# Kernel optimization log

Measured on AMD Instinct MI355X. Metric: run time of the kernel, lower is better.

The kernel has to match this reference:

```python
import jax, jax.numpy as jnp
import numpy as np


def _gcn_conv(x, src, dst, norm, W, b, n_nodes):
    # PyG GCNConv: transform then normalized scatter-add aggregation.
    h = x @ W                                        # [N, F_out]
    msg = h[src] * norm[:, None]                     # [E+N, F_out] gather
    out = jax.ops.segment_sum(msg, dst, num_segments=n_nodes)  # scatter-add
    return out + b


def setup_inputs() -> dict:
    key = jax.random.key(0)
    ks = jax.random.split(key, 8)
    N, E, F_in, H, C = 100000, 1000000, 128, 64, 40
    x = jax.random.normal(ks[0], (N, F_in), dtype=jnp.float32)
    edge_index = jax.random.randint(ks[1], (2, E), 0, N, dtype=jnp.int64)
    W1 = jax.random.normal(ks[2], (F_in, H), dtype=jnp.float32) * (1.0 / np.sqrt(F_in))
    b1 = jnp.zeros((H,), jnp.float32)
    W2 = jax.random.normal(ks[3], (H, H), dtype=jnp.float32) * (1.0 / np.sqrt(H))
    b2 = jnp.zeros((H,), jnp.float32)
    Wc = jax.random.normal(ks[4], (H, C), dtype=jnp.float32) * (1.0 / np.sqrt(H))
    bc = jnp.zeros((C,), jnp.float32)
    return {"x": x, "edge_index": edge_index, "W1": W1, "b1": b1,
            "W2": W2, "b2": b2, "Wc": Wc, "bc": bc}


def reference(x, edge_index, W1, b1, W2, b2, Wc, bc):
    n_nodes = x.shape[0]
    # Add self loops (GCNConv default), symmetric normalization.
    loop = jnp.arange(n_nodes, dtype=edge_index.dtype)
    src = jnp.concatenate([edge_index[0], loop])
    dst = jnp.concatenate([edge_index[1], loop])
    deg = jax.ops.segment_sum(jnp.ones_like(dst, jnp.float32), dst,
                              num_segments=n_nodes)
    dinv = jnp.where(deg > 0, jax.lax.rsqrt(jnp.maximum(deg, 1.0)), 0.0)
    norm = dinv[src] * dinv[dst]                     # [E+N]

    h = jax.nn.relu(_gcn_conv(x, src, dst, norm, W1, b1, n_nodes))
    # dropout: identity (inference / training=False)
    h = jax.nn.relu(_gcn_conv(h, src, dst, norm, W2, b2, n_nodes))
    return h @ Wc + bc                               # [N, out_dim]
```

## Files before the change

kernel.cpp:

```cpp
#include <hip/hip_runtime.h>
#include <hip/hip_fp16.h>


#define BUCKET_BITS  8
#define BUCKET_NODES 256
#define MAXB 512
#define CAP  8192
#define OFF_MASK 0x3FFFFF

typedef _Float16 half8 __attribute__((ext_vector_type(8)));
typedef float    f32x4 __attribute__((ext_vector_type(4)));

union H8  { uint4 u; __half h[8]; };
union HV8 { uint4 u; half8 h; };

__global__ void zero_kernel(int* __restrict__ p, int n) {
    int i = blockIdx.x * blockDim.x + threadIdx.x;
    if (i < n) p[i] = 0;
}

__global__ __launch_bounds__(256) void bucket_fill_kernel(const int* __restrict__ src,
                                                          const int* __restrict__ dst,
                                                          int* __restrict__ bucketCursor,
                                                          unsigned int* __restrict__ bucketArr,
                                                          int E, int NB) {
    __shared__ int lcnt[MAXB];
    __shared__ int dcache[4096];
    for (int i = threadIdx.x; i < NB; i += 256) lcnt[i] = 0;
    __syncthreads();
    const int base = blockIdx.x * 4096;
#pragma unroll
    for (int k = 0; k < 16; ++k) {
        int idx = k * 256 + threadIdx.x;
        int e = base + idx;
        if (e < E) {
            int d = dst[e];
            dcache[idx] = d;
            atomicAdd(&lcnt[d >> BUCKET_BITS], 1);
        }
    }
    __syncthreads();
    for (int i = threadIdx.x; i < NB; i += 256) {
        int c = lcnt[i];
        if (c) lcnt[i] = i * CAP + atomicAdd(&bucketCursor[i], c);
    }
    __syncthreads();
#pragma unroll
    for (int k = 0; k < 16; ++k) {
        int idx = k * 256 + threadIdx.x;
        int e = base + idx;
        if (e < E) {
            int d = dcache[idx];
            int s = src[e];
            int pos = atomicAdd(&lcnt[d >> BUCKET_BITS], 1);
            bucketArr[pos] = ((unsigned)(d & (BUCKET_NODES - 1)) << 24) | (unsigned)s;
        }
    }
}

__global__ __launch_bounds__(256) void node_sort_kernel(const unsigned int* __restrict__ bucketArr,
                                                        const int* __restrict__ bucketCursor,
                                                        unsigned int* __restrict__ nodeInfo,
                                                        float* __restrict__ dinv,
                                                        unsigned int* __restrict__ adj, int N) {
    __shared__ int cnt[BUCKET_NODES];
    __shared__ int scn[BUCKET_NODES];
    __shared__ int cur[BUCKET_NODES];
    const int t = threadIdx.x;
    const int b = blockIdx.x;
    cnt[t] = 0;
    __syncthreads();
    const int e0 = b * CAP;
    const int e1 = e0 + bucketCursor[b];
    for (int e = e0 + t; e < e1; e += 256)
        atomicAdd(&cnt[bucketArr[e] >> 24], 1);
    __syncthreads();
    int v = cnt[t];
    scn[t] = v;
    __syncthreads();
    for (int off = 1; off < 256; off <<= 1) {
        int u = (t >= off) ? scn[t - off] : 0;
        __syncthreads();
        scn[t] += u;
        __syncthreads();
    }
    const int excl = scn[t] - v;
    const int node = b * BUCKET_NODES + t;
    if (node < N) {
        nodeInfo[node] = ((unsigned)v << 22) | (unsigned)(e0 + excl);
        dinv[node]     = rsqrtf((float)(v + 1));
    }
    cur[t] = e0 + excl;
    __syncthreads();
    for (int e = e0 + t; e < e1; e += 256) {
        unsigned int entry = bucketArr[e];
        int pos = atomicAdd(&cur[entry >> 24], 1);
        adj[pos] = entry & 0xFFFFFF;
    }
}

template <int K, int NOUT, int NCT, bool AHALF, bool OHALF, bool SCALE, bool BIAS>
__global__ __launch_bounds__(256) void gemm_mfma(const void* __restrict__ Av,
                                                 const float* __restrict__ W,
                                                 const float* __restrict__ bias,
                                                 const float* __restrict__ dscale,
                                                 void* __restrict__ outv, int M) {
    constexpr int KP = K + 8;
    __shared__ _Float16 WTh[64 * KP];
    __shared__ _Float16 WTl[64 * KP];

    for (int i = threadIdx.x; i < K * 64; i += 256) {
        int k = i >> 6, c = i & 63;
        float w = (NOUT == 64 || c < NOUT) ? W[k * NOUT + c] : 0.f;
        _Float16 h = (_Float16)w;
        WTh[c * KP + k] = h;
        WTl[c * KP + k] = (_Float16)(w - (float)h);
    }
    __syncthreads();

    const int lane = threadIdx.x & 63;
    const int wv   = threadIdx.x >> 6;
    const int r    = lane & 15;
    const int q    = lane >> 4;
    int arow = blockIdx.x * 64 + wv * 16 + r;
    if (arow > M - 1) arow = M - 1;

    f32x4 acc[NCT] = {};

#pragma unroll
    for (int kst = 0; kst < K; kst += 32) {
        half8 ah = {}, al = {};
        if (AHALF) {
            HV8 v;
            v.u = *(const uint4*)((const __half*)Av + (size_t)arow * K + kst + q * 8);
            ah = v.h;
        } else {
            const float* ap = (const float*)Av + (size_t)arow * K + kst + q * 8;
            float4 f0 = *(const float4*)ap;
            float4 f1 = *(const float4*)(ap + 4);
            float fs[8] = {f0.x, f0.y, f0.z, f0.w, f1.x, f1.y, f1.z, f1.w};
#pragma unroll
            for (int j = 0; j < 8; ++j) {
                _Float16 h = (_Float16)fs[j];
                ah[j] = h;
                al[j] = (_Float16)(fs[j] - (float)h);
            }
        }
#pragma unroll
        for (int n = 0; n < NCT; ++n) {
            const int bo = (n * 16 + r) * KP + kst + q * 8;
            HV8 bh, bl;
            bh.u = *(const uint4*)(WTh + bo);
            bl.u = *(const uint4*)(WTl + bo);
            acc[n] = __builtin_amdgcn_mfma_f32_16x16x32_f16(ah, bh.h, acc[n], 0, 0, 0);
            acc[n] = __builtin_amdgcn_mfma_f32_16x16x32_f16(ah, bl.h, acc[n], 0, 0, 0);
            if (!AHALF)
                acc[n] = __builtin_amdgcn_mfma_f32_16x16x32_f16(al, bh.h, acc[n], 0, 0, 0);
        }
    }

    const int orow0 = blockIdx.x * 64 + wv * 16 + q * 4;
#pragma unroll
    for (int n = 0; n < NCT; ++n) {
        const int col = n * 16 + r;
        float bb = 0.f;
        if (BIAS) bb = (col < NOUT) ? bias[col] : 0.f;
#pragma unroll
        for (int j = 0; j < 4; ++j) {
            const int row = orow0 + j;
            if (row >= M) break;
            const float sc = SCALE ? dscale[row] : 1.f;
            const float v = acc[n][j] * sc + bb;
            if (OHALF) {
                ((__half*)outv)[(size_t)row * NOUT + col] = __float2half(v);
            } else if (col < NOUT) {
                ((float*)outv)[(size_t)row * NOUT + col] = v;
            }
        }
    }
}

__global__ __launch_bounds__(256) void gather_kernel(const __half* __restrict__ h,
                                                     const unsigned int* __restrict__ nodeInfo,
                                                     const unsigned int* __restrict__ adj,
                                                     const float* __restrict__ dinv,
                                                     const float* __restrict__ bias,
                                                     __half* __restrict__ out, int N) {
    const int node = blockIdx.x * 32 + (threadIdx.x >> 3);
    const int o    = (threadIdx.x >> 3) & 7;
    const int l    = threadIdx.x & 7;
    if (node >= N) return;

    const unsigned info = nodeInfo[node];
    const int start = (int)(info & OFF_MASK);
    const int end   = start + (int)(info >> 22);
    const float di  = dinv[node];

    float acc[8];
    {
        H8 sv;
        sv.u = *(const uint4*)(h + (size_t)node * 64 + l * 8);
#pragma unroll
        for (int k = 0; k < 8; ++k) acc[k] = __half2float(sv.h[k]);
    }

    for (int base = start; ; base += 8) {
        bool active = base < end;
        if (__ballot(active) == 0ull) break;
        int m = 0;
        int sidx = 0;
        if (active) {
            m = min(8, end - base);
            if (l < m) sidx = (int)adj[base + l];
        }
#pragma unroll
        for (int j = 0; j < 8; ++j) {
            if (j < m) {
                int s = __shfl(sidx, (o << 3) | j);
                H8 rv;
                rv.u = *(const uint4*)(h + (size_t)s * 64 + l * 8);
#pragma unroll
                for (int k = 0; k < 8; ++k) acc[k] += __half2float(rv.h[k]);
            }
        }
    }

    const float4 b0 = *(const float4*)(bias + l * 8);
    const float4 b1 = *(const float4*)(bias + l * 8 + 4);
    const float bb[8] = {b0.x, b0.y, b0.z, b0.w, b1.x, b1.y, b1.z, b1.w};
    H8 ov;
#pragma unroll
    for (int k = 0; k < 8; ++k) {
        float v = acc[k] * di + bb[k];
        ov.h[k] = __float2half(v > 0.f ? v : 0.f);
    }
    *(uint4*)(out + (size_t)node * 64 + l * 8) = ov.u;
}

extern "C" void kernel_launch(void* const* d_in, const int* in_sizes, int n_in,
                              void* d_out, int out_size, void* d_ws, size_t ws_size,
                              hipStream_t stream) {
    const float* x  = (const float*)d_in[0];
    const int*   ei = (const int*)d_in[1];
    const float* W1 = (const float*)d_in[2];
    const float* b1 = (const float*)d_in[3];
    const float* W2 = (const float*)d_in[4];
    const float* b2 = (const float*)d_in[5];
    const float* Wc = (const float*)d_in[6];
    const float* bc = (const float*)d_in[7];

    const int N = in_sizes[0] / 128;
    const int E = in_sizes[1] / 2;
    const int* src = ei;
    const int* dst = ei + E;

    const int NB = (N + BUCKET_NODES - 1) >> BUCKET_BITS;
    const int EB = (E + 4095) / 4096;

    char* w = (char*)d_ws;
    auto alloc = [&](size_t bytes) { char* p = w; w += (bytes + 255) & ~(size_t)255; return p; };
    int*          bucketCursor = (int*)alloc((size_t)NB * 4);
    unsigned int* bucketArr    = (unsigned int*)alloc((size_t)NB * CAP * 4);
    unsigned int* nodeInfo     = (unsigned int*)alloc((size_t)N * 4);
    unsigned int* adj          = (unsigned int*)alloc((size_t)NB * CAP * 4);
    float*        dinv         = (float*)alloc((size_t)N * 4);
    __half*       bufA         = (__half*)alloc((size_t)N * 64 * 2);
    __half*       bufB         = (__half*)alloc((size_t)N * 64 * 2);

    dim3 blk(256);
    const int nblkG = (N + 63) / 64;
    const int nblkV = (N + 31) / 32;

    zero_kernel<<<(NB + 255) / 256, blk, 0, stream>>>(bucketCursor, NB);
    bucket_fill_kernel<<<EB, blk, 0, stream>>>(src, dst, bucketCursor, bucketArr, E, NB);
    node_sort_kernel<<<NB, blk, 0, stream>>>(bucketArr, bucketCursor, nodeInfo, dinv, adj, N);

    gemm_mfma<128, 64, 4, false, true, true, false><<<nblkG, blk, 0, stream>>>(
        x, W1, nullptr, dinv, bufA, N);
    gather_kernel<<<nblkV, blk, 0, stream>>>(bufA, nodeInfo, adj, dinv, b1, bufB, N);

    gemm_mfma<64, 64, 4, true, true, true, false><<<nblkG, blk, 0, stream>>>(
        bufB, W2, nullptr, dinv, bufA, N);
    gather_kernel<<<nblkV, blk, 0, stream>>>(bufA, nodeInfo, adj, dinv, b2, bufB, N);

    gemm_mfma<64, 40, 3, true, false, false, true><<<nblkG, blk, 0, stream>>>(
        bufB, Wc, bc, nullptr, d_out, N);
}
```

Before: 222.2 us.

## Fuse neighbor aggregation with following dense transform into one kernel

Replaces the separate gather kernels and the subsequent GEMMs with a single gather_gemm kernel. Each block aggregates neighbor features for 64 nodes into shared memory, then multiplies by the next layer's weights using MFMA with a split-fp16 (high/low) weight representation. This removes the intermediate fp16 round trip through global memory and two kernel launches. In exchange, each thread handles two nodes serially and reads adjacency indices directly instead of through shuffles, which may reduce gather parallelism and occupancy because of the larger shared-memory footprint.

```diff
diff --git a/kernel.cpp b/kernel.cpp
--- a/kernel.cpp
+++ b/kernel.cpp
@@ -180,61 +180,117 @@
     }
 }
 
-__global__ __launch_bounds__(256) void gather_kernel(const __half* __restrict__ h,
-                                                     const unsigned int* __restrict__ nodeInfo,
-                                                     const unsigned int* __restrict__ adj,
-                                                     const float* __restrict__ dinv,
-                                                     const float* __restrict__ bias,
-                                                     __half* __restrict__ out, int N) {
-    const int node = blockIdx.x * 32 + (threadIdx.x >> 3);
-    const int o    = (threadIdx.x >> 3) & 7;
+template <int NOUT, int NCT, bool OHALF, bool SCALE, bool OBIAS>
+__global__ __launch_bounds__(256) void gather_gemm(const __half* __restrict__ h,
+                                                   const unsigned int* __restrict__ nodeInfo,
+                                                   const unsigned int* __restrict__ adj,
+                                                   const float* __restrict__ dinv,
+                                                   const float* __restrict__ gbias,
+                                                   const float* __restrict__ W,
+                                                   const float* __restrict__ obias,
+                                                   void* __restrict__ outv, int N) {
+    constexpr int KP = 72;
+    __shared__ _Float16 At[64 * KP];
+    __shared__ _Float16 WTh[64 * KP];
+    __shared__ _Float16 WTl[64 * KP];
+
+    for (int i = threadIdx.x; i < 64 * 64; i += 256) {
+        int k = i >> 6, c = i & 63;
+        float w = (NOUT == 64 || c < NOUT) ? W[k * NOUT + c] : 0.f;
+        _Float16 hh = (_Float16)w;
+        WTh[c * KP + k] = hh;
+        WTl[c * KP + k] = (_Float16)(w - (float)hh);
+    }
+
+    const int row0 = blockIdx.x * 64;
+    const int E8   = threadIdx.x >> 3;
     const int l    = threadIdx.x & 7;
-    if (node >= N) return;
-
-    const unsigned info = nodeInfo[node];
-    const int start = (int)(info & OFF_MASK);
-    const int end   = start + (int)(info >> 22);
-    const float di  = dinv[node];
-
-    float acc[8];
-    {
-        H8 sv;
-        sv.u = *(const uint4*)(h + (size_t)node * 64 + l * 8);
-#pragma unroll
-        for (int k = 0; k < 8; ++k) acc[k] = __half2float(sv.h[k]);
-    }
-
-    for (int base = start; ; base += 8) {
-        bool active = base < end;
-        if (__ballot(active) == 0ull) break;
-        int m = 0;
-        int sidx = 0;
-        if (active) {
-            m = min(8, end - base);
-            if (l < m) sidx = (int)adj[base + l];
-        }
-#pragma unroll
-        for (int j = 0; j < 8; ++j) {
-            if (j < m) {
-                int s = __shfl(sidx, (o << 3) | j);
-                H8 rv;
-                rv.u = *(const uint4*)(h + (size_t)s * 64 + l * 8);
-#pragma unroll
-                for (int k = 0; k < 8; ++k) acc[k] += __half2float(rv.h[k]);
+
+    const float4 g0 = *(const float4*)(gbias + l * 8);
+    const float4 g1 = *(const float4*)(gbias + l * 8 + 4);
+    const float gb[8] = {g0.x, g0.y, g0.z, g0.w, g1.x, g1.y, g1.z, g1.w};
+
+#pragma unroll
+    for (int half = 0; half < 2; ++half) {
+        const int lr = E8 + half * 32;
+        int node = row0 + lr;
+        if (node > N - 1) node = N - 1;
+        const unsigned info = nodeInfo[node];
+        const int start = (int)(info & OFF_MASK);
+        const int end   = start + (int)(info >> 22);
+        const float di  = dinv[node];
+
+        float acc[8];
+        {
+            H8 sv;
+            sv.u = *(const uint4*)(h + (size_t)node * 64 + l * 8);
+#pragma unroll
+            for (int k = 0; k < 8; ++k) acc[k] = __half2float(sv.h[k]);
+        }
+        for (int base = start; base < end; base += 8) {
+            const int m = min(8, end - base);
+            int idx[8];
+#pragma unroll
+            for (int j = 0; j < 8; ++j) idx[j] = (int)adj[base + j];
+#pragma unroll
+            for (int j = 0; j < 8; ++j)
+                if (j < m) {
+                    H8 rv;
+                    rv.u = *(const uint4*)(h + (size_t)idx[j] * 64 + l * 8);
+#pragma unroll
+                    for (int k = 0; k < 8; ++k) acc[k] += __half2float(rv.h[k]);
+                }
+        }
+        H8 ov;
+#pragma unroll
+        for (int k = 0; k < 8; ++k) {
+            float v = acc[k] * di + gb[k];
+            ov.h[k] = __float2half(v > 0.f ? v : 0.f);
+        }
+        *(uint4*)(&At[lr * KP + l * 8]) = ov.u;
+    }
+    __syncthreads();
+
+    const int lane = threadIdx.x & 63;
+    const int wv   = threadIdx.x >> 6;
+    const int r    = lane & 15;
+    const int q    = lane >> 4;
+
+    f32x4 acc2[NCT] = {};
+#pragma unroll
+    for (int kst = 0; kst < 64; kst += 32) {
+        HV8 av;
+        av.u = *(const uint4*)(&At[(wv * 16 + r) * KP + kst + q * 8]);
+#pragma unroll
+        for (int n = 0; n < NCT; ++n) {
+            const int bo = (n * 16 + r) * KP + kst + q * 8;
+            HV8 bh, bl;
+            bh.u = *(const uint4*)(&WTh[bo]);
+            bl.u = *(const uint4*)(&WTl[bo]);
+            acc2[n] = __builtin_amdgcn_mfma_f32_16x16x32_f16(av.h, bh.h, acc2[n], 0, 0, 0);
+            acc2[n] = __builtin_amdgcn_mfma_f32_16x16x32_f16(av.h, bl.h, acc2[n], 0, 0, 0);
+        }
+    }
+
+    const int orow0 = row0 + wv * 16 + q * 4;
+#pragma unroll
+    for (int n = 0; n < NCT; ++n) {
+        const int col = n * 16 + r;
+        float bb = 0.f;
+        if (OBIAS) bb = (col < NOUT) ? obias[col] : 0.f;
+#pragma unroll
+        for (int j = 0; j < 4; ++j) {
+            const int row = orow0 + j;
+            if (row >= N) break;
+            const float sc = SCALE ? dinv[row] : 1.f;
+            const float v = acc2[n][j] * sc + bb;
+            if (OHALF) {
+                ((__half*)outv)[(size_t)row * NOUT + col] = __float2half(v);
+            } else if (col < NOUT) {
+                ((float*)outv)[(size_t)row * NOUT + col] = v;
             }
         }
     }
-
-    const float4 b0 = *(const float4*)(bias + l * 8);
-    const float4 b1 = *(const float4*)(bias + l * 8 + 4);
-    const float bb[8] = {b0.x, b0.y, b0.z, b0.w, b1.x, b1.y, b1.z, b1.w};
-    H8 ov;
-#pragma unroll
-    for (int k = 0; k < 8; ++k) {
-        float v = acc[k] * di + bb[k];
-        ov.h[k] = __float2half(v > 0.f ? v : 0.f);
-    }
-    *(uint4*)(out + (size_t)node * 64 + l * 8) = ov.u;
 }
 
 extern "C" void kernel_launch(void* const* d_in, const int* in_sizes, int n_in,
@@ -269,7 +325,6 @@
 
     dim3 blk(256);
     const int nblkG = (N + 63) / 64;
-    const int nblkV = (N + 31) / 32;
 
     zero_kernel<<<(NB + 255) / 256, blk, 0, stream>>>(bucketCursor, NB);
     bucket_fill_kernel<<<EB, blk, 0, stream>>>(src, dst, bucketCursor, bucketArr, E, NB);
@@ -277,12 +332,10 @@
 
     gemm_mfma<128, 64, 4, false, true, true, false><<<nblkG, blk, 0, stream>>>(
         x, W1, nullptr, dinv, bufA, N);
-    gather_kernel<<<nblkV, blk, 0, stream>>>(bufA, nodeInfo, adj, dinv, b1, bufB, N);
-
-    gemm_mfma<64, 64, 4, true, true, true, false><<<nblkG, blk, 0, stream>>>(
-        bufB, W2, nullptr, dinv, bufA, N);
-    gather_kernel<<<nblkV, blk, 0, stream>>>(bufA, nodeInfo, adj, dinv, b2, bufB, N);
-
-    gemm_mfma<64, 40, 3, true, false, false, true><<<nblkG, blk, 0, stream>>>(
-        bufB, Wc, bc, nullptr, d_out, N);
-}
+
+    gather_gemm<64, 4, true, true, false><<<nblkG, blk, 0, stream>>>(
+        bufA, nodeInfo, adj, dinv, b1, W2, nullptr, bufB, N);
+
+    gather_gemm<40, 3, false, false, true><<<nblkG, blk, 0, stream>>>(
+        bufB, nodeInfo, adj, dinv, b2, Wc, bc, d_out, N);
+}
```

Result: slower. 232.2 us (+4.5%).
